# Performance work log

Measured on AMD Instinct MI355X. Metric: run time of the kernel, lower is better.

The kernel has to match this reference:

```python
import jax, jax.numpy as jnp
import numpy as np

TEMPERATURE = 0.1
EPS = 1e-12  # tf.math.l2_normalize epsilon

BATCH = 512
DIM = 256
QUEUE = 65536


def l2_normalize(x, axis=1):
    sq = jnp.sum(x * x, axis=axis, keepdims=True)
    return x * jax.lax.rsqrt(jnp.maximum(sq, EPS))


def setup_inputs() -> dict:
    key = jax.random.key(0)
    k1, k2, k3 = jax.random.split(key, 3)
    projections_1 = jax.random.normal(k1, (BATCH, DIM), dtype=jnp.float32)
    projections_2 = jax.random.normal(k2, (BATCH, DIM), dtype=jnp.float32)
    feature_queue = l2_normalize(jax.random.normal(k3, (QUEUE, DIM), dtype=jnp.float32), axis=1)
    return {"projections_1": projections_1, "projections_2": projections_2, "feature_queue": feature_queue}


def nearest_neighbour(projections, feature_queue):
    # [B, Q] similarity vs the memory queue, 1-NN retrieval + gather
    support_similarities = jnp.einsum('bd,qd->bq', projections, feature_queue)
    nn_idx = jnp.argmax(support_similarities, axis=1)
    nn_projections = feature_queue[nn_idx]  # [B, D]
    # straight-through: forward value is nn, gradient flows to projections
    return projections + jax.lax.stop_gradient(nn_projections - projections)


def reference(projections_1, projections_2, feature_queue):
    p1 = l2_normalize(projections_1, axis=1)
    p2 = l2_normalize(projections_2, axis=1)

    nn1 = nearest_neighbour(p1, feature_queue)
    nn2 = nearest_neighbour(p2, feature_queue)

    s_1_2_1 = jnp.einsum('bd,cd->bc', nn1, p2) / TEMPERATURE
    s_1_2_2 = jnp.einsum('bd,cd->bc', p2, nn1) / TEMPERATURE
    s_2_1_1 = jnp.einsum('bd,cd->bc', nn2, p1) / TEMPERATURE
    s_2_1_2 = jnp.einsum('bd,cd->bc', p1, nn2) / TEMPERATURE

    logits = jnp.concatenate([s_1_2_1, s_1_2_2, s_2_1_1, s_2_1_2], axis=0)  # [4B, B]
    batch = p1.shape[0]
    labels = jnp.tile(jnp.arange(batch), 4)  # [4B]

    # sparse categorical crossentropy from logits
    logp = jax.nn.log_softmax(logits, axis=-1)
    loss = -logp[jnp.arange(4 * batch), labels]  # [4B]

    # FIFO queue update (normalized projections_1 pushed in front)
    new_queue = jnp.concatenate([p1, feature_queue[:-batch]], axis=0)
    return loss, new_queue
```

## Files before the change

kernel.cpp:

```cpp
#include <hip/hip_runtime.h>
#include <stdint.h>


#define BATCH  512
#define DIM    256
#define QUEUE  65536
#define MROWS  1024
#define NGRP   2048
#define MARGIN 0.01f

typedef short bf16x8 __attribute__((ext_vector_type(8)));
typedef float f32x4  __attribute__((ext_vector_type(4)));

__device__ __forceinline__ unsigned int mono_f32(float f) {
    unsigned int u = __float_as_uint(f);
    return (u & 0x80000000u) ? ~u : (u | 0x80000000u);
}
__device__ __forceinline__ float unmono_f32(unsigned int m) {
    unsigned int u = (m & 0x80000000u) ? (m ^ 0x80000000u) : ~m;
    return __uint_as_float(u);
}
__device__ __forceinline__ unsigned short f2bf(float f) {
    unsigned int u = __float_as_uint(f);
    return (unsigned short)((u + 0x7fffu + ((u >> 16) & 1u)) >> 16);
}

__global__ void k1_norm(const float* __restrict__ p1, const float* __restrict__ p2,
                        float* __restrict__ Pn, float* __restrict__ PnT,
                        unsigned short* __restrict__ PhiF, float* __restrict__ outq,
                        int* __restrict__ npairs, unsigned int* __restrict__ rowmaxU,
                        unsigned long long* __restrict__ rowfinal)
{
    const int r = blockIdx.x;
    const int t = threadIdx.x;
    if (t == 0) {
        rowmaxU[r] = 0u;
        rowfinal[r] = 0ull;
        if (r == 0) *npairs = 0;
    }
    const float* src = (r < BATCH) ? p1 : p2;
    const int row = (r < BATCH) ? r : r - BATCH;
    float4 v = ((const float4*)(src + (size_t)row * DIM))[t];
    float sq = v.x*v.x + v.y*v.y + v.z*v.z + v.w*v.w;
    #pragma unroll
    for (int off = 32; off; off >>= 1) sq += __shfl_xor(sq, off, 64);
    sq = fmaxf(sq, 1e-12f);
    float s = rsqrtf(sq);
    s = s * (1.5f - 0.5f * sq * s * s);
    v.x *= s; v.y *= s; v.z *= s; v.w *= s;
    ((float4*)(Pn + (size_t)r * DIM))[t] = v;
    const int k = t * 4;
    PnT[(size_t)(k + 0) * MROWS + r] = v.x;
    PnT[(size_t)(k + 1) * MROWS + r] = v.y;
    PnT[(size_t)(k + 2) * MROWS + r] = v.z;
    PnT[(size_t)(k + 3) * MROWS + r] = v.w;
    short4 b;
    b.x = (short)f2bf(v.x); b.y = (short)f2bf(v.y);
    b.z = (short)f2bf(v.z); b.w = (short)f2bf(v.w);
    {
        const int c = t >> 1;
        const int idx = ((r >> 4) * 8 + (c >> 2)) * 64 + (c & 3) * 16 + (r & 15);
        *(short4*)((char*)PhiF + (size_t)idx * 16 + (t & 1) * 8) = b;
    }
    if (r < BATCH) ((float4*)(outq + (size_t)r * DIM))[t] = v;
}

__global__ __launch_bounds__(256)
void k0_prep(const float* __restrict__ queue, float* __restrict__ outq,
             char* __restrict__ Qbf)
{
    const int b = blockIdx.x;
    const int t = threadIdx.x;
    const int n0 = b * 32;
    const f32x4* qsrc = (const f32x4*)(queue + (size_t)n0 * DIM);
    f32x4* qdst = (f32x4*)(outq + (size_t)(n0 + BATCH) * DIM);
    char* tile = Qbf + (size_t)(b >> 1) * 32768;

    f32x4 va[8];
    #pragma unroll
    for (int it = 0; it < 4; ++it) {
        const int L = it * 256 + t;
        const int r = L >> 5, c16 = L & 31;
        va[2 * it]     = qsrc[(size_t)r * 64 + c16 * 2];
        va[2 * it + 1] = qsrc[(size_t)r * 64 + c16 * 2 + 1];
    }
    #pragma unroll
    for (int it = 0; it < 4; ++it) {
        const int L = it * 256 + t;
        const int r = L >> 5, c16 = L & 31;
        f32x4 v0 = va[2 * it], v1 = va[2 * it + 1];
        if (n0 + r < QUEUE - BATCH) {
            qdst[(size_t)r * 64 + c16 * 2]     = v0;
            qdst[(size_t)r * 64 + c16 * 2 + 1] = v1;
        }
        bf16x8 bb;
        bb[0] = (short)f2bf(v0.x); bb[1] = (short)f2bf(v0.y);
        bb[2] = (short)f2bf(v0.z); bb[3] = (short)f2bf(v0.w);
        bb[4] = (short)f2bf(v1.x); bb[5] = (short)f2bf(v1.y);
        bb[6] = (short)f2bf(v1.z); bb[7] = (short)f2bf(v1.w);
        const int rr = ((b & 1) << 5) + r;
        *(bf16x8*)(tile + rr * 512 + ((c16 ^ (rr & 31)) << 4)) = bb;
    }
}

__device__ __forceinline__ void k2_stage_async(const char* __restrict__ tile,
                                               char* Bsb, int t)
{
    #pragma unroll
    for (int it = 0; it < 8; ++it) {
        const int L = it * 256 + t;
        __builtin_amdgcn_global_load_lds(
            (const __attribute__((address_space(1))) unsigned int*)(tile + (size_t)L * 16),
            (__attribute__((address_space(3))) unsigned int*)(Bsb + L * 16), 16, 0, 0);
    }
}

__global__ __launch_bounds__(256, 2)
void k2_mfma(const unsigned short* __restrict__ PhiF, const char* __restrict__ Qbf,
             float* __restrict__ cand, unsigned int* __restrict__ rowmaxU)
{
    __shared__ __align__(16) char Bs[2][32768];
    const int bid = blockIdx.x;
    const int c = (bid >> 5) * 8 + (bid & 7);
    const int s = (bid >> 3) & 3;
    const int t  = threadIdx.x;
    const int w  = t >> 6, lane = t & 63;
    const int lr = lane & 15, q = lane >> 4;
    const int mbase = s * 256 + w * 64;
    const char* chunkbase = Qbf + (size_t)(c * 4) * 32768;

    bf16x8 pfr[4][8];
    {
        const char* Pw = (const char*)PhiF;
        const int mt16b = mbase >> 4;
        #pragma unroll
        for (int mj = 0; mj < 4; ++mj)
            #pragma unroll
            for (int ks = 0; ks < 8; ++ks)
                pfr[mj][ks] = *(const bf16x8*)(Pw + ((size_t)((mt16b + mj) * 8 + ks) * 64 + lane) * 16);
    }

    k2_stage_async(chunkbase, Bs[0], t);
    __syncthreads();

    float rowmx[4] = {-1e30f, -1e30f, -1e30f, -1e30f};

    for (int tl = 0; tl < 4; ++tl) {
        if (tl < 3)
            k2_stage_async(chunkbase + (size_t)(tl + 1) * 32768, Bs[(tl + 1) & 1], t);

        char* Bsb = Bs[tl & 1];
        f32x4 acc[4][4];
        #pragma unroll
        for (int i = 0; i < 4; ++i)
            #pragma unroll
            for (int j = 0; j < 4; ++j) acc[i][j] = (f32x4){0.f, 0.f, 0.f, 0.f};

        #pragma unroll
        for (int ks = 0; ks < 8; ++ks) {
            bf16x8 qf[4];
            #pragma unroll
            for (int ni = 0; ni < 4; ++ni) {
                const int r = ni * 16 + lr;
                const int c16 = ks * 4 + q;
                qf[ni] = *(const bf16x8*)(Bsb + r * 512 + ((c16 ^ (r & 31)) << 4));
            }
            #pragma unroll
            for (int ni = 0; ni < 4; ++ni)
                #pragma unroll
                for (int mj = 0; mj < 4; ++mj)
                    acc[ni][mj] = __builtin_amdgcn_mfma_f32_16x16x32_bf16(qf[ni], pfr[mj][ks], acc[ni][mj], 0, 0, 0);
        }

        #pragma unroll
        for (int mj = 0; mj < 4; ++mj) {
            #pragma unroll
            for (int gl = 0; gl < 2; ++gl) {
                f32x4 va = acc[2 * gl][mj], vb = acc[2 * gl + 1][mj];
                float mx = fmaxf(fmaxf(fmaxf(va[0], va[1]), fmaxf(va[2], va[3])),
                                 fmaxf(fmaxf(vb[0], vb[1]), fmaxf(vb[2], vb[3])));
                mx = fmaxf(mx, __shfl_xor(mx, 16, 64));
                mx = fmaxf(mx, __shfl_xor(mx, 32, 64));
                rowmx[mj] = fmaxf(rowmx[mj], mx);
                if (q == 0)
                    cand[(size_t)(c * 8 + tl * 2 + gl) * MROWS + (mbase + mj * 16 + lr)] = mx;
            }
        }
        __syncthreads();
    }

    if (q == 0) {
        #pragma unroll
        for (int mj = 0; mj < 4; ++mj)
            atomicMax(rowmaxU + mbase + mj * 16 + lr, mono_f32(rowmx[mj]));
    }
}

__global__ void k2c_filter(const float* __restrict__ cand, const unsigned int* __restrict__ rowmaxU,
                           unsigned int* __restrict__ pairs, int* __restrict__ npairs)
{
    const int t  = threadIdx.x;
    const int ml = t & 63, gs = t >> 6;
    const int mc = blockIdx.x & 15, gc = blockIdx.x >> 4;
    const int m  = mc * 64 + ml;
    const int g0 = gc * 128 + gs * 32;
    const float thr = unmono_f32(rowmaxU[m]) - MARGIN;
    #pragma unroll 8
    for (int j = 0; j < 32; ++j) {
        if (cand[(size_t)(g0 + j) * MROWS + m] >= thr) {
            int p = atomicAdd(npairs, 1);
            pairs[p] = ((unsigned int)m << 16) | (unsigned int)(g0 + j);
        }
    }
}

__global__ __launch_bounds__(256, 4)
void k2d_rescore(const unsigned int* __restrict__ pairs, const int* __restrict__ npairs,
                 const float* __restrict__ Pn, const float* __restrict__ queue,
                 unsigned long long* __restrict__ rowfinal)
{
    const int t = threadIdx.x, w = t >> 6, lane = t & 63;
    const int n = *npairs;
    const int col_l = lane & 31, half = lane >> 5;
    for (int p = blockIdx.x * 4 + w; p < n; p += gridDim.x * 4) {
        const unsigned int pr = pairs[p];
        const int row = pr >> 16, g = pr & 0xffff;
        const int col = g * 32 + col_l;
        const float4* qp = (const float4*)(queue + (size_t)col * DIM + half * 128);
        const float4* pp = (const float4*)(Pn + (size_t)row * DIM + half * 128);
        float4 sv = {0.f, 0.f, 0.f, 0.f};
        #pragma unroll 8
        for (int j = 0; j < 32; ++j) {
            float4 a = pp[j], b = qp[j];
            sv.x = fmaf(a.x, b.x, sv.x); sv.y = fmaf(a.y, b.y, sv.y);
            sv.z = fmaf(a.z, b.z, sv.z); sv.w = fmaf(a.w, b.w, sv.w);
        }
        float s = (sv.x + sv.y) + (sv.z + sv.w);
        s += __shfl_xor(s, 32, 64);
        unsigned long long best = ((unsigned long long)mono_f32(s) << 32)
                                | (unsigned int)(65535 - col);
        #pragma unroll
        for (int off = 1; off <= 16; off <<= 1) {
            unsigned long long o = __shfl_xor(best, off, 64);
            best = best > o ? best : o;
        }
        if (lane == 0) atomicMax(rowfinal + row, best);
    }
}

__global__ void k3_sim(const unsigned long long* __restrict__ rowfinal,
                       const float* __restrict__ queue,
                       const float* __restrict__ PnT, float* __restrict__ S)
{
    const int b  = blockIdx.x;
    const int rb = (b >> 1) * 8;
    const int ch = b & 1;
    const int tid = threadIdx.x;
    const int which = (rb < BATCH) ? 0 : 1;
    const int colbase = which ? 0 : BATCH;
    const int col = colbase + ch * 256 + tid;
    __shared__ float nnv[8][DIM];
    #pragma unroll
    for (int j = 0; j < 8; ++j) {
        const int idx = 65535 - (int)(rowfinal[rb + j] & 0xFFFFull);
        nnv[j][tid] = queue[(size_t)idx * DIM + tid];
    }
    __syncthreads();
    float acc[8];
    #pragma unroll
    for (int j = 0; j < 8; ++j) acc[j] = 0.f;
    for (int k4 = 0; k4 < 64; ++k4) {
        float4 nv[8];
        #pragma unroll
        for (int j = 0; j < 8; ++j) nv[j] = ((const float4*)nnv[j])[k4];
        #pragma unroll
        for (int kk = 0; kk < 4; ++kk) {
            const int k = k4 * 4 + kk;
            const float v0 = PnT[(size_t)k * MROWS + col];
            #pragma unroll
            for (int j = 0; j < 8; ++j) {
                const float nj = ((const float*)&nv[j])[kk];
                acc[j] = fmaf(nj, v0, acc[j]);
            }
        }
    }
    const int i0 = rb & (BATCH - 1);
    float* Sout = S + (size_t)which * (BATCH * BATCH);
    #pragma unroll
    for (int j = 0; j < 8; ++j)
        Sout[(size_t)(i0 + j) * BATCH + ch * 256 + tid] = acc[j] * 10.0f;
}

__global__ void k4_loss(const float* __restrict__ S, float* __restrict__ loss)
{
    const int r = blockIdx.x;
    const int tid = threadIdx.x;
    const int grp = r >> 9;
    const int i = r & 511;
    const float* M = S + (size_t)(grp >> 1) * (BATCH * BATCH);
    float x0, x1;
    if (!(grp & 1)) { x0 = M[(size_t)i * BATCH + tid];  x1 = M[(size_t)i * BATCH + tid + 256]; }
    else            { x0 = M[(size_t)tid * BATCH + i];  x1 = M[(size_t)(tid + 256) * BATCH + i]; }
    const float diag = M[(size_t)i * BATCH + i];
    float mx = fmaxf(x0, x1);
    #pragma unroll
    for (int off = 1; off < 64; off <<= 1) mx = fmaxf(mx, __shfl_xor(mx, off, 64));
    __shared__ float redm[4], reds[4];
    if ((tid & 63) == 0) redm[tid >> 6] = mx;
    __syncthreads();
    mx = fmaxf(fmaxf(redm[0], redm[1]), fmaxf(redm[2], redm[3]));
    float e = __expf(x0 - mx) + __expf(x1 - mx);
    #pragma unroll
    for (int off = 1; off < 64; off <<= 1) e += __shfl_xor(e, off, 64);
    if ((tid & 63) == 0) reds[tid >> 6] = e;
    __syncthreads();
    if (tid == 0)
        loss[r] = mx + logf(reds[0] + reds[1] + reds[2] + reds[3]) - diag;
}

extern "C" void kernel_launch(void* const* d_in, const int* in_sizes, int n_in,
                              void* d_out, int out_size, void* d_ws, size_t ws_size,
                              hipStream_t stream)
{
    const float* p1    = (const float*)d_in[0];
    const float* p2    = (const float*)d_in[1];
    const float* queue = (const float*)d_in[2];
    float* out  = (float*)d_out;
    float* loss = out;
    float* outq = out + 4 * BATCH;

    char* w = (char*)d_ws;
    float* cand = (float*)w;                               w += (size_t)NGRP * MROWS * 4;
    unsigned long long* rowfinal = (unsigned long long*)w; w += MROWS * 8;
    unsigned int* rowmaxU = (unsigned int*)w;              w += MROWS * 4;
    float* Pn  = (float*)w;                                w += (size_t)MROWS * DIM * 4;
    float* PnT = (float*)w;                                w += (size_t)MROWS * DIM * 4;
    unsigned short* PhiF = (unsigned short*)w;             w += (size_t)MROWS * DIM * 2;
    float* S = (float*)w;                                  w += (size_t)2 * BATCH * BATCH * 4;
    int* npairs = (int*)w;                                 w += 16;
    char* Qbf = w;
    unsigned int* pairs = (unsigned int*)Qbf;

    hipLaunchKernelGGL(k1_norm,     dim3(MROWS), dim3(64),  0, stream, p1, p2, Pn, PnT, PhiF, outq,
                       npairs, rowmaxU, rowfinal);
    hipLaunchKernelGGL(k0_prep,     dim3(QUEUE / 32), dim3(256), 0, stream, queue, outq, Qbf);
    hipLaunchKernelGGL(k2_mfma,     dim3(1024), dim3(256), 0, stream, PhiF, Qbf, cand, rowmaxU);
    hipLaunchKernelGGL(k2c_filter,  dim3(256),   dim3(256), 0, stream, cand, rowmaxU, pairs, npairs);
    hipLaunchKernelGGL(k2d_rescore, dim3(512),   dim3(256), 0, stream, pairs, npairs, Pn, queue, rowfinal);
    hipLaunchKernelGGL(k3_sim,      dim3(256),   dim3(256), 0, stream, rowfinal, queue, PnT, S);
    hipLaunchKernelGGL(k4_loss,     dim3(4 * BATCH), dim3(256), 0, stream, S, loss);
}
```

Baseline: 232.3 us.

## Fuse prep kernels and filter+rescore into single launches; halve k3 rows per block

Merges the normalization and queue-prep kernels into one launch using a block-index split. The candidate filter and the rescore step become a single kernel that gathers hits in shared memory with block-local atomics, which removes the global pair list and global counter. k3_sim now handles 4 rows per block instead of 8 and launches twice as many blocks. The aim is to cut launch count, global atomics and serialization; the risk is that a block with many hits rescores them serially and the shared hit buffer could overflow.

```diff
diff --git a/kernel.cpp b/kernel.cpp
--- a/kernel.cpp
+++ b/kernel.cpp
@@ -25,81 +25,80 @@
     return (unsigned short)((u + 0x7fffu + ((u >> 16) & 1u)) >> 16);
 }
 
-__global__ void k1_norm(const float* __restrict__ p1, const float* __restrict__ p2,
-                        float* __restrict__ Pn, float* __restrict__ PnT,
-                        unsigned short* __restrict__ PhiF, float* __restrict__ outq,
-                        int* __restrict__ npairs, unsigned int* __restrict__ rowmaxU,
-                        unsigned long long* __restrict__ rowfinal)
-{
-    const int r = blockIdx.x;
+__global__ __launch_bounds__(256)
+void k01_prep(const float* __restrict__ queue, float* __restrict__ outq,
+              char* __restrict__ Qbf,
+              const float* __restrict__ p1, const float* __restrict__ p2,
+              float* __restrict__ Pn, float* __restrict__ PnT,
+              unsigned short* __restrict__ PhiF,
+              unsigned int* __restrict__ rowmaxU, unsigned long long* __restrict__ rowfinal)
+{
+    const int bid = blockIdx.x;
     const int t = threadIdx.x;
-    if (t == 0) {
-        rowmaxU[r] = 0u;
-        rowfinal[r] = 0ull;
-        if (r == 0) *npairs = 0;
-    }
-    const float* src = (r < BATCH) ? p1 : p2;
-    const int row = (r < BATCH) ? r : r - BATCH;
-    float4 v = ((const float4*)(src + (size_t)row * DIM))[t];
-    float sq = v.x*v.x + v.y*v.y + v.z*v.z + v.w*v.w;
-    #pragma unroll
-    for (int off = 32; off; off >>= 1) sq += __shfl_xor(sq, off, 64);
-    sq = fmaxf(sq, 1e-12f);
-    float s = rsqrtf(sq);
-    s = s * (1.5f - 0.5f * sq * s * s);
-    v.x *= s; v.y *= s; v.z *= s; v.w *= s;
-    ((float4*)(Pn + (size_t)r * DIM))[t] = v;
-    const int k = t * 4;
-    PnT[(size_t)(k + 0) * MROWS + r] = v.x;
-    PnT[(size_t)(k + 1) * MROWS + r] = v.y;
-    PnT[(size_t)(k + 2) * MROWS + r] = v.z;
-    PnT[(size_t)(k + 3) * MROWS + r] = v.w;
-    short4 b;
-    b.x = (short)f2bf(v.x); b.y = (short)f2bf(v.y);
-    b.z = (short)f2bf(v.z); b.w = (short)f2bf(v.w);
-    {
-        const int c = t >> 1;
-        const int idx = ((r >> 4) * 8 + (c >> 2)) * 64 + (c & 3) * 16 + (r & 15);
-        *(short4*)((char*)PhiF + (size_t)idx * 16 + (t & 1) * 8) = b;
-    }
-    if (r < BATCH) ((float4*)(outq + (size_t)r * DIM))[t] = v;
-}
-
-__global__ __launch_bounds__(256)
-void k0_prep(const float* __restrict__ queue, float* __restrict__ outq,
-             char* __restrict__ Qbf)
-{
-    const int b = blockIdx.x;
-    const int t = threadIdx.x;
-    const int n0 = b * 32;
-    const f32x4* qsrc = (const f32x4*)(queue + (size_t)n0 * DIM);
-    f32x4* qdst = (f32x4*)(outq + (size_t)(n0 + BATCH) * DIM);
-    char* tile = Qbf + (size_t)(b >> 1) * 32768;
-
-    f32x4 va[8];
-    #pragma unroll
-    for (int it = 0; it < 4; ++it) {
-        const int L = it * 256 + t;
-        const int r = L >> 5, c16 = L & 31;
-        va[2 * it]     = qsrc[(size_t)r * 64 + c16 * 2];
-        va[2 * it + 1] = qsrc[(size_t)r * 64 + c16 * 2 + 1];
-    }
-    #pragma unroll
-    for (int it = 0; it < 4; ++it) {
-        const int L = it * 256 + t;
-        const int r = L >> 5, c16 = L & 31;
-        f32x4 v0 = va[2 * it], v1 = va[2 * it + 1];
-        if (n0 + r < QUEUE - BATCH) {
-            qdst[(size_t)r * 64 + c16 * 2]     = v0;
-            qdst[(size_t)r * 64 + c16 * 2 + 1] = v1;
-        }
-        bf16x8 bb;
-        bb[0] = (short)f2bf(v0.x); bb[1] = (short)f2bf(v0.y);
-        bb[2] = (short)f2bf(v0.z); bb[3] = (short)f2bf(v0.w);
-        bb[4] = (short)f2bf(v1.x); bb[5] = (short)f2bf(v1.y);
-        bb[6] = (short)f2bf(v1.z); bb[7] = (short)f2bf(v1.w);
-        const int rr = ((b & 1) << 5) + r;
-        *(bf16x8*)(tile + rr * 512 + ((c16 ^ (rr & 31)) << 4)) = bb;
+
+    if (bid < 2048) {
+        const int n0 = bid * 32;
+        const f32x4* qsrc = (const f32x4*)(queue + (size_t)n0 * DIM);
+        f32x4* qdst = (f32x4*)(outq + (size_t)(n0 + BATCH) * DIM);
+        char* tile = Qbf + (size_t)(bid >> 1) * 32768;
+
+        f32x4 va[8];
+        #pragma unroll
+        for (int it = 0; it < 4; ++it) {
+            const int L = it * 256 + t;
+            const int r = L >> 5, c16 = L & 31;
+            va[2 * it]     = qsrc[(size_t)r * 64 + c16 * 2];
+            va[2 * it + 1] = qsrc[(size_t)r * 64 + c16 * 2 + 1];
+        }
+        #pragma unroll
+        for (int it = 0; it < 4; ++it) {
+            const int L = it * 256 + t;
+            const int r = L >> 5, c16 = L & 31;
+            f32x4 v0 = va[2 * it], v1 = va[2 * it + 1];
+            if (n0 + r < QUEUE - BATCH) {
+                qdst[(size_t)r * 64 + c16 * 2]     = v0;
+                qdst[(size_t)r * 64 + c16 * 2 + 1] = v1;
+            }
+            bf16x8 bb;
+            bb[0] = (short)f2bf(v0.x); bb[1] = (short)f2bf(v0.y);
+            bb[2] = (short)f2bf(v0.z); bb[3] = (short)f2bf(v0.w);
+            bb[4] = (short)f2bf(v1.x); bb[5] = (short)f2bf(v1.y);
+            bb[6] = (short)f2bf(v1.z); bb[7] = (short)f2bf(v1.w);
+            const int rr = ((bid & 1) << 5) + r;
+            *(bf16x8*)(tile + rr * 512 + ((c16 ^ (rr & 31)) << 4)) = bb;
+        }
+    } else {
+        const int sub = t >> 6, lane = t & 63;
+        const int r = (bid - 2048) * 4 + sub;
+        if (lane == 0) {
+            rowmaxU[r] = 0u;
+            rowfinal[r] = 0ull;
+        }
+        const float* src = (r < BATCH) ? p1 : p2;
+        const int row = (r < BATCH) ? r : r - BATCH;
+        float4 v = ((const float4*)(src + (size_t)row * DIM))[lane];
+        float sq = v.x*v.x + v.y*v.y + v.z*v.z + v.w*v.w;
+        #pragma unroll
+        for (int off = 32; off; off >>= 1) sq += __shfl_xor(sq, off, 64);
+        sq = fmaxf(sq, 1e-12f);
+        float s = rsqrtf(sq);
+        s = s * (1.5f - 0.5f * sq * s * s);
+        v.x *= s; v.y *= s; v.z *= s; v.w *= s;
+        ((float4*)(Pn + (size_t)r * DIM))[lane] = v;
+        const int k = lane * 4;
+        PnT[(size_t)(k + 0) * MROWS + r] = v.x;
+        PnT[(size_t)(k + 1) * MROWS + r] = v.y;
+        PnT[(size_t)(k + 2) * MROWS + r] = v.z;
+        PnT[(size_t)(k + 3) * MROWS + r] = v.w;
+        short4 b;
+        b.x = (short)f2bf(v.x); b.y = (short)f2bf(v.y);
+        b.z = (short)f2bf(v.z); b.w = (short)f2bf(v.w);
+        {
+            const int c = lane >> 1;
+            const int idx = ((r >> 4) * 8 + (c >> 2)) * 64 + (c & 3) * 16 + (r & 15);
+            *(short4*)((char*)PhiF + (size_t)idx * 16 + (lane & 1) * 8) = b;
+        }
+        if (r < BATCH) ((float4*)(outq + (size_t)r * DIM))[lane] = v;
     }
 }
 
@@ -196,34 +195,38 @@
     }
 }
 
-__global__ void k2c_filter(const float* __restrict__ cand, const unsigned int* __restrict__ rowmaxU,
-                           unsigned int* __restrict__ pairs, int* __restrict__ npairs)
-{
-    const int t  = threadIdx.x;
-    const int ml = t & 63, gs = t >> 6;
-    const int mc = blockIdx.x & 15, gc = blockIdx.x >> 4;
-    const int m  = mc * 64 + ml;
-    const int g0 = gc * 128 + gs * 32;
-    const float thr = unmono_f32(rowmaxU[m]) - MARGIN;
-    #pragma unroll 8
-    for (int j = 0; j < 32; ++j) {
-        if (cand[(size_t)(g0 + j) * MROWS + m] >= thr) {
-            int p = atomicAdd(npairs, 1);
-            pairs[p] = ((unsigned int)m << 16) | (unsigned int)(g0 + j);
-        }
-    }
-}
-
-__global__ __launch_bounds__(256, 4)
-void k2d_rescore(const unsigned int* __restrict__ pairs, const int* __restrict__ npairs,
-                 const float* __restrict__ Pn, const float* __restrict__ queue,
-                 unsigned long long* __restrict__ rowfinal)
-{
-    const int t = threadIdx.x, w = t >> 6, lane = t & 63;
-    const int n = *npairs;
+__global__ __launch_bounds__(256)
+void k2cd(const float* __restrict__ cand, const unsigned int* __restrict__ rowmaxU,
+          const float* __restrict__ Pn, const float* __restrict__ queue,
+          unsigned long long* __restrict__ rowfinal)
+{
+    __shared__ unsigned int hits[8192];
+    __shared__ int nhits;
+    const int t = threadIdx.x;
+    if (t == 0) nhits = 0;
+    __syncthreads();
+
+    {
+        const int ml = t & 63, gs = t >> 6;
+        const int mc = blockIdx.x & 15, gc = blockIdx.x >> 4;
+        const int m  = mc * 64 + ml;
+        const int g0 = gc * 128 + gs * 32;
+        const float thr = unmono_f32(rowmaxU[m]) - MARGIN;
+        #pragma unroll 8
+        for (int j = 0; j < 32; ++j) {
+            if (cand[(size_t)(g0 + j) * MROWS + m] >= thr) {
+                int p = atomicAdd(&nhits, 1);
+                hits[p] = ((unsigned int)m << 16) | (unsigned int)(g0 + j);
+            }
+        }
+    }
+    __syncthreads();
+
+    const int n = nhits;
+    const int w = t >> 6, lane = t & 63;
     const int col_l = lane & 31, half = lane >> 5;
-    for (int p = blockIdx.x * 4 + w; p < n; p += gridDim.x * 4) {
-        const unsigned int pr = pairs[p];
+    for (int p = w; p < n; p += 4) {
+        const unsigned int pr = hits[p];
         const int row = pr >> 16, g = pr & 0xffff;
         const int col = g * 32 + col_l;
         const float4* qp = (const float4*)(queue + (size_t)col * DIM + half * 128);
@@ -253,32 +256,32 @@
                        const float* __restrict__ PnT, float* __restrict__ S)
 {
     const int b  = blockIdx.x;
-    const int rb = (b >> 1) * 8;
+    const int rb = (b >> 1) * 4;
     const int ch = b & 1;
     const int tid = threadIdx.x;
     const int which = (rb < BATCH) ? 0 : 1;
     const int colbase = which ? 0 : BATCH;
     const int col = colbase + ch * 256 + tid;
-    __shared__ float nnv[8][DIM];
-    #pragma unroll
-    for (int j = 0; j < 8; ++j) {
+    __shared__ float nnv[4][DIM];
+    #pragma unroll
+    for (int j = 0; j < 4; ++j) {
         const int idx = 65535 - (int)(rowfinal[rb + j] & 0xFFFFull);
         nnv[j][tid] = queue[(size_t)idx * DIM + tid];
     }
     __syncthreads();
-    float acc[8];
-    #pragma unroll
-    for (int j = 0; j < 8; ++j) acc[j] = 0.f;
+    float acc[4];
+    #pragma unroll
+    for (int j = 0; j < 4; ++j) acc[j] = 0.f;
     for (int k4 = 0; k4 < 64; ++k4) {
-        float4 nv[8];
-        #pragma unroll
-        for (int j = 0; j < 8; ++j) nv[j] = ((const float4*)nnv[j])[k4];
+        float4 nv[4];
+        #pragma unroll
+        for (int j = 0; j < 4; ++j) nv[j] = ((const float4*)nnv[j])[k4];
         #pragma unroll
         for (int kk = 0; kk < 4; ++kk) {
             const int k = k4 * 4 + kk;
             const float v0 = PnT[(size_t)k * MROWS + col];
             #pragma unroll
-            for (int j = 0; j < 8; ++j) {
+            for (int j = 0; j < 4; ++j) {
                 const float nj = ((const float*)&nv[j])[kk];
                 acc[j] = fmaf(nj, v0, acc[j]);
             }
@@ -287,7 +290,7 @@
     const int i0 = rb & (BATCH - 1);
     float* Sout = S + (size_t)which * (BATCH * BATCH);
     #pragma unroll
-    for (int j = 0; j < 8; ++j)
+    for (int j = 0; j < 4; ++j)
         Sout[(size_t)(i0 + j) * BATCH + ch * 256 + tid] = acc[j] * 10.0f;
 }
 
@@ -337,16 +340,12 @@
     float* PnT = (float*)w;                                w += (size_t)MROWS * DIM * 4;
     unsigned short* PhiF = (unsigned short*)w;             w += (size_t)MROWS * DIM * 2;
     float* S = (float*)w;                                  w += (size_t)2 * BATCH * BATCH * 4;
-    int* npairs = (int*)w;                                 w += 16;
     char* Qbf = w;
-    unsigned int* pairs = (unsigned int*)Qbf;
-
-    hipLaunchKernelGGL(k1_norm,     dim3(MROWS), dim3(64),  0, stream, p1, p2, Pn, PnT, PhiF, outq,
-                       npairs, rowmaxU, rowfinal);
-    hipLaunchKernelGGL(k0_prep,     dim3(QUEUE / 32), dim3(256), 0, stream, queue, outq, Qbf);
+
+    hipLaunchKernelGGL(k01_prep,    dim3(2048 + 256), dim3(256), 0, stream,
+                       queue, outq, Qbf, p1, p2, Pn, PnT, PhiF, rowmaxU, rowfinal);
     hipLaunchKernelGGL(k2_mfma,     dim3(1024), dim3(256), 0, stream, PhiF, Qbf, cand, rowmaxU);
-    hipLaunchKernelGGL(k2c_filter,  dim3(256),   dim3(256), 0, stream, cand, rowmaxU, pairs, npairs);
-    hipLaunchKernelGGL(k2d_rescore, dim3(512),   dim3(256), 0, stream, pairs, npairs, Pn, queue, rowfinal);
-    hipLaunchKernelGGL(k3_sim,      dim3(256),   dim3(256), 0, stream, rowfinal, queue, PnT, S);
+    hipLaunchKernelGGL(k2cd,        dim3(256),  dim3(256), 0, stream, cand, rowmaxU, Pn, queue, rowfinal);
+    hipLaunchKernelGGL(k3_sim,      dim3(512),  dim3(256), 0, stream, rowfinal, queue, PnT, S);
     hipLaunchKernelGGL(k4_loss,     dim3(4 * BATCH), dim3(256), 0, stream, S, loss);
 }
```

Result: faster. 213.7 us (-8.0%).
